# Optimization experiments

Hardware: AMD Instinct MI355X
Metric: run time of the kernel (lower is better)

## Reference

```python
import jax, jax.numpy as jnp
import numpy as np

N_STEPS = 5
STATE_DIM = 512
ANN_DIM = 256
N_NODES = 2048
N_EDGE_TYPES = 4


def setup_inputs() -> dict:
    key = jax.random.key(0)
    ks = jax.random.split(key, 12)
    D, E, N = STATE_DIM, N_EDGE_TYPES, N_NODES
    s = 0.02
    adjacency = (jax.random.uniform(ks[0], (N, N * 2 * E)) < 0.015).astype(jnp.float32)
    annotations = jax.random.normal(ks[1], (N, ANN_DIM), dtype=jnp.float32)
    W_prop = jax.random.normal(ks[2], (2 * E, D, D), dtype=jnp.float32) * s
    b_prop = jnp.zeros((2 * E, D), dtype=jnp.float32)
    Wz = jax.random.normal(ks[3], (D, D), dtype=jnp.float32) * s
    Uz = jax.random.normal(ks[4], (D, D), dtype=jnp.float32) * s
    bz = jnp.zeros((D,), dtype=jnp.float32)
    Wr = jax.random.normal(ks[5], (D, D), dtype=jnp.float32) * s
    Ur = jax.random.normal(ks[6], (D, D), dtype=jnp.float32) * s
    br = jnp.zeros((D,), dtype=jnp.float32)
    Wh = jax.random.normal(ks[7], (D, D), dtype=jnp.float32) * s
    Uh = jax.random.normal(ks[8], (D, D), dtype=jnp.float32) * s
    bh = jnp.zeros((D,), dtype=jnp.float32)
    return dict(adjacency=adjacency, annotations=annotations, W_prop=W_prop, b_prop=b_prop,
                Wz=Wz, Uz=Uz, bz=bz, Wr=Wr, Ur=Ur, br=br, Wh=Wh, Uh=Uh, bh=bh)


def reference(adjacency, annotations, W_prop, b_prop, Wz, Uz, bz, Wr, Ur, br, Wh, Uh, bh):
    N = annotations.shape[0]
    D = W_prop.shape[-1]
    # pad annotations into first columns of state (input1[:, :ann_dim] = annotations)
    h = jnp.zeros((N, D), dtype=annotations.dtype).at[:, :annotations.shape[1]].set(annotations)
    for _ in range(N_STEPS):
        # per-edge-type linear transforms: edge_type_list [2E, N, D]
        t = jnp.einsum('nd,edf->enf', h, W_prop) + b_prop[:, None, :]
        # adjacency aggregation: A is [N, N*2E] with per-edge-type column blocks
        a = adjacency @ t.reshape(-1, D)  # [N, D]
        # GRU node update (UpdateNet)
        z = jax.nn.sigmoid(a @ Wz + h @ Uz + bz)
        r = jax.nn.sigmoid(a @ Wr + h @ Ur + br)
        h_tilde = jnp.tanh(a @ Wh + (r * h) @ Uh + bh)
        h = (1.0 - z) * h + z * h_tilde
    return h
```

## Files before the change

### kernel.cpp

```cpp
#include <hip/hip_runtime.h>

typedef __attribute__((ext_vector_type(8))) short short8;
typedef __attribute__((ext_vector_type(4))) float floatx4;

#define NSTEPS 5
#define DD 512
#define ANN 256
#define NNODE 2048
#define NEDGE 8
#define NCOLS (NNODE * NEDGE)
#define MAXE 96
#define KP (NEDGE * DD)


typedef __attribute__((address_space(3))) unsigned lds_u32;
typedef const __attribute__((address_space(1))) unsigned g_u32;
__device__ __forceinline__ void gload16(const short* g, short* l) {
    __builtin_amdgcn_global_load_lds((g_u32*)g, (lds_u32*)l, 16, 0, 0);
}

__device__ inline float bf2f(unsigned short s) {
    unsigned u = ((unsigned)s) << 16;
    float f; __builtin_memcpy(&f, &u, 4);
    return f;
}
__device__ inline unsigned short f2bf(float f) {
    unsigned u; __builtin_memcpy(&u, &f, 4);
    u += 0x7fffu + ((u >> 16) & 1u);
    return (unsigned short)(u >> 16);
}
__device__ inline void split2(float x, unsigned short& hi, unsigned short& lo) {
    hi = f2bf(x);
    lo = f2bf(x - bf2f(hi));
}
__device__ inline void fo_write(short* __restrict__ Fhi, short* __restrict__ Flo,
                                int row, int col, float v) {
    unsigned short hs, ls;
    split2(v, hs, ls);
    size_t a = ((size_t)(row >> 4) * 64 + (col >> 3)) * 128 + ((row & 15) << 3) + (col & 7);
    Fhi[a] = (short)hs;
    Flo[a] = (short)ls;
}
__device__ inline void fo_write2(short* __restrict__ Fhi, short* __restrict__ Flo,
                                 int row, int c, float v0, float v1) {
    unsigned short h0, l0, h1, l1;
    split2(v0, h0, l0);
    split2(v1, h1, l1);
    size_t a = ((size_t)(row >> 4) * 64 + (c >> 3)) * 128 + ((row & 15) << 3) + (c & 7);
    *(unsigned*)(Fhi + a) = (unsigned)h0 | ((unsigned)h1 << 16);
    *(unsigned*)(Flo + a) = (unsigned)l0 | ((unsigned)l1 << 16);
}

__global__ __launch_bounds__(256) void k_init(const float* __restrict__ ann,
                                              float* __restrict__ h,
                                              short* __restrict__ HBhi,
                                              short* __restrict__ HBlo,
                                              int* __restrict__ cnt2) {
    int n = blockIdx.x, t = threadIdx.x;
    int c = 2 * t;
    float v0 = 0.f, v1 = 0.f;
    if (c < ANN) {
        v0 = ann[(size_t)n * ANN + c];
        v1 = ann[(size_t)n * ANN + c + 1];
    }
    h[(size_t)n * DD + c]     = v0;
    h[(size_t)n * DD + c + 1] = v1;
    fo_write2(HBhi, HBlo, n, c, v0, v1);
    if (t < NEDGE) cnt2[n * NEDGE + t] = 0;
}

__global__ __launch_bounds__(256) void k_build(const float* __restrict__ adj,
                                               int* __restrict__ cnt2,
                                               unsigned short* __restrict__ idx) {
    int n = blockIdx.x;
    const float* row = adj + (size_t)n * NCOLS;
    for (int j8 = threadIdx.x; j8 < NCOLS / 8; j8 += 256) {
        floatx4 a = *(const floatx4*)(row + j8 * 8);
        floatx4 b = *(const floatx4*)(row + j8 * 8 + 4);
        unsigned nz = 0;
        #pragma unroll
        for (int i = 0; i < 4; i++) {
            if (a[i] != 0.f) nz |= 1u << i;
            if (b[i] != 0.f) nz |= 1u << (4 + i);
        }
        while (nz) {
            int i = __builtin_ctz(nz);
            nz &= nz - 1;
            int j = j8 * 8 + i;
            int e = j >> 11;
            int m = j & (NNODE - 1);
            int p = atomicAdd(&cnt2[n * NEDGE + e], 1);
            if (p < MAXE) idx[((size_t)n * NEDGE + e) * MAXE + p] = (unsigned short)m;
        }
    }
}

__global__ __launch_bounds__(256) void k_transP(const float* __restrict__ W,
                                                short* __restrict__ Fhi,
                                                short* __restrict__ Flo, int K) {
    __shared__ float st[32][33];
    int tx = threadIdx.x & 31, ty = threadIdx.x >> 5;
    int k0 = blockIdx.x * 32, n0 = blockIdx.y * 32;
    #pragma unroll
    for (int i = 0; i < 4; i++)
        st[ty + i * 8][tx] = W[(size_t)(k0 + ty + i * 8) * DD + n0 + tx];
    __syncthreads();
    #pragma unroll
    for (int i = 0; i < 4; i++) {
        int n = n0 + ty + i * 8, k = k0 + tx;
        float v = st[tx][ty + i * 8];
        unsigned short hs, ls;
        split2(v, hs, ls);
        size_t a = ((size_t)(n >> 4) * (K >> 3) + (k >> 3)) * 128 + ((n & 15) << 3) + (k & 7);
        Fhi[a] = (short)hs;
        Flo[a] = (short)ls;
    }
}

__global__ __launch_bounds__(256) void k_transG(const float* __restrict__ s00,
                                                const float* __restrict__ s10,
                                                const float* __restrict__ s01,
                                                const float* __restrict__ s11,
                                                short* __restrict__ Fhi,
                                                short* __restrict__ Flo) {
    __shared__ float st[32][33];
    const int K = 2 * DD;
    int tx = threadIdx.x & 31, ty = threadIdx.x >> 5;
    int k0 = blockIdx.x * 32, n0 = blockIdx.y * 32;
    const float* sk0 = (n0 < DD) ? s00 : s01;
    const float* sk1 = (n0 < DD) ? s10 : s11;
    #pragma unroll
    for (int i = 0; i < 4; i++) {
        int k = k0 + ty + i * 8;
        const float* s = (k < DD) ? sk0 : sk1;
        st[ty + i * 8][tx] = s[(size_t)(k & (DD - 1)) * DD + ((n0 + tx) & (DD - 1))];
    }
    __syncthreads();
    #pragma unroll
    for (int i = 0; i < 4; i++) {
        int n = n0 + ty + i * 8, k = k0 + tx;
        float v = st[tx][ty + i * 8];
        unsigned short hs, ls;
        split2(v, hs, ls);
        size_t a = ((size_t)(n >> 4) * (K >> 3) + (k >> 3)) * 128 + ((n & 15) << 3) + (k & 7);
        Fhi[a] = (short)hs;
        Flo[a] = (short)ls;
    }
}

__global__ __launch_bounds__(256) void k_gather_all(const float* __restrict__ h,
                                                    const int* __restrict__ cnt2,
                                                    const unsigned short* __restrict__ idx,
                                                    const float* __restrict__ bp,
                                                    short* __restrict__ Gbhi,
                                                    short* __restrict__ Gblo,
                                                    float* __restrict__ abuf) {
    __shared__ unsigned short sidx[NEDGE * MAXE];
    __shared__ int scnt[NEDGE];
    int n = blockIdx.x, t = threadIdx.x;

    if (t < NEDGE) scnt[t] = cnt2[n * NEDGE + t];
    for (int j = t; j < NEDGE * MAXE / 2; j += 256)
        ((unsigned*)sidx)[j] = ((const unsigned*)(idx + (size_t)n * NEDGE * MAXE))[j];
    __syncthreads();

    const int th = t & 127;
    const int eg = t >> 7;
    size_t wbase = ((size_t)(n >> 4) * 512) * 128 + ((n & 15) << 3) + ((th & 1) << 2);

    #pragma unroll 1
    for (int ee = 0; ee < 4; ee++) {
        int e = eg * 4 + ee;
        int raw = scnt[e];
        int m = raw > MAXE ? MAXE : raw;
        const unsigned short* row = &sidx[e * MAXE];
        floatx4 a0 = (floatx4){0.f, 0.f, 0.f, 0.f};
        floatx4 a1 = (floatx4){0.f, 0.f, 0.f, 0.f};
        int i = 0;
        for (; i + 16 <= m; i += 16) {
            #pragma unroll
            for (int j = 0; j < 8; j++) {
                a0 += *(const floatx4*)(h + (size_t)row[i + j] * DD + 4 * th);
                a1 += *(const floatx4*)(h + (size_t)row[i + 8 + j] * DD + 4 * th);
            }
        }
        if (i + 8 <= m) {
            #pragma unroll
            for (int j = 0; j < 8; j++)
                a0 += *(const floatx4*)(h + (size_t)row[i + j] * DD + 4 * th);
            i += 8;
        }
        if (i + 4 <= m) {
            #pragma unroll
            for (int j = 0; j < 4; j++)
                a1 += *(const floatx4*)(h + (size_t)row[i + j] * DD + 4 * th);
            i += 4;
        }
        for (; i < m; i++)
            a0 += *(const floatx4*)(h + (size_t)row[i] * DD + 4 * th);
        floatx4 a = a0 + a1;

        unsigned short hs[4], ls[4];
        #pragma unroll
        for (int j = 0; j < 4; j++) split2(a[j], hs[j], ls[j]);
        unsigned long long hp = (unsigned long long)hs[0] | ((unsigned long long)hs[1] << 16)
                              | ((unsigned long long)hs[2] << 32) | ((unsigned long long)hs[3] << 48);
        unsigned long long lp = (unsigned long long)ls[0] | ((unsigned long long)ls[1] << 16)
                              | ((unsigned long long)ls[2] << 32) | ((unsigned long long)ls[3] << 48);
        size_t addr = wbase + (size_t)(e * 64 + (th >> 1)) * 128;
        __builtin_nontemporal_store(hp, (unsigned long long*)(Gbhi + addr));
        __builtin_nontemporal_store(lp, (unsigned long long*)(Gblo + addr));
    }

    if (eg == 0) {
        floatx4 s = (floatx4){0.f, 0.f, 0.f, 0.f};
        #pragma unroll
        for (int e = 0; e < NEDGE; e++)
            s += (float)scnt[e] * *(const floatx4*)(bp + e * DD + 4 * th);
        __builtin_nontemporal_store(s, (floatx4*)(abuf + (size_t)n * DD + 4 * th));
    }
}

template<int MODE>
__global__ __launch_bounds__(256, 4) void k_gemm8(
    const short* __restrict__ A0hi, const short* __restrict__ A0lo,
    const short* __restrict__ A1hi, const short* __restrict__ A1lo,
    const short* __restrict__ Bhi,  const short* __restrict__ Blo,
    const float* __restrict__ bias0, const float* __restrict__ bias1,
    float* __restrict__ zbuf,
    float* __restrict__ h,
    short* __restrict__ Ohi, short* __restrict__ Olo,
    float* __restrict__ P0, float* __restrict__ P1) {

    __shared__ short S[24][512];

    const int tid = threadIdx.x;
    const int lane = tid & 63;
    const int wave = tid >> 6;
    const int wm = wave >> 1;
    const int wn = wave & 1;
    const int quad = lane >> 4;
    const int l16 = lane & 15;

    const int pbid = blockIdx.x;
    const int x = pbid & 7;
    const int j = pbid >> 3;
    const int mband = x * 4 + (j & 3);
    int kh, bx;
    if (MODE == 1) { kh = 0; bx = j >> 2; }
    else           { kh = (j >> 2) & 1; bx = j >> 3; }
    const int blockM = mband * 64;
    const int blockN = bx * 32;
    const int mt0 = blockM >> 4, nt0 = blockN >> 4;
    const int KCB = (MODE == 0) ? 512 : 128;
    const int bko = (MODE == 0) ? kh * 256 : (MODE == 2 ? kh * 64 : 0);
    const int Kloc = (MODE == 0) ? 2048 : (MODE == 1 ? 1024 : 512);

    const short* Ahi_s = (MODE == 2 && kh) ? A1hi : A0hi;
    const short* Alo_s = (MODE == 2 && kh) ? A1lo : A0lo;

    floatx4 acc[2];
    acc[0] = (floatx4){0.f, 0.f, 0.f, 0.f};
    acc[1] = (floatx4){0.f, 0.f, 0.f, 0.f};

    auto gaddr = [&](int k0, int s) -> const short* {
        if (s < 16) {
            int pl = s >> 3, u = s & 7;
            int mt = u >> 1, ks = u & 1;
            const short* base;
            int kc, stride;
            if (MODE == 0) {
                base = pl ? A0lo : A0hi;
                kc = kh * 256 + (k0 >> 3) + ks * 4;
                stride = 512;
            } else if (MODE == 1) {
                int seg = k0 >> 9;
                base = seg ? (pl ? A1lo : A1hi) : (pl ? A0lo : A0hi);
                kc = ((k0 & 511) >> 3) + ks * 4;
                stride = 64;
            } else {
                base = pl ? Alo_s : Ahi_s;
                kc = (k0 >> 3) + ks * 4;
                stride = 64;
            }
            return base + ((size_t)(mt0 + mt) * stride + kc) * 128;
        } else {
            int u = s - 16, pl = u >> 2, ks = (u >> 1) & 1, nt = u & 1;
            const short* base = pl ? Blo : Bhi;
            return base + ((size_t)(nt0 + nt) * KCB + bko + (k0 >> 3) + ks * 4) * 128;
        }
    };

    for (int k0 = 0; k0 < Kloc; k0 += 64) {
        #pragma unroll
        for (int jj = 0; jj < 6; jj++) {
            int s = jj * 4 + wave;
            gload16(gaddr(k0, s) + lane * 8, &S[s][lane * 8]);
        }
        __syncthreads();

        #pragma unroll
        for (int ks = 0; ks < 2; ks++) {
            short8 ah[2], al[2], bh, bl;
            #pragma unroll
            for (int mi = 0; mi < 2; mi++) {
                ah[mi] = *(const short8*)&S[(wm * 2 + mi) * 2 + ks][lane * 8];
                al[mi] = *(const short8*)&S[8 + (wm * 2 + mi) * 2 + ks][lane * 8];
            }
            bh = *(const short8*)&S[16 + ks * 2 + wn][lane * 8];
            bl = *(const short8*)&S[20 + ks * 2 + wn][lane * 8];
            #pragma unroll
            for (int mi = 0; mi < 2; mi++) {
                acc[mi] = __builtin_amdgcn_mfma_f32_16x16x32_bf16(ah[mi], bh, acc[mi], 0, 0, 0);
                acc[mi] = __builtin_amdgcn_mfma_f32_16x16x32_bf16(ah[mi], bl, acc[mi], 0, 0, 0);
                acc[mi] = __builtin_amdgcn_mfma_f32_16x16x32_bf16(al[mi], bh, acc[mi], 0, 0, 0);
            }
        }
        __syncthreads();
    }

    float* P = kh ? P1 : P0;
    #pragma unroll
    for (int mi = 0; mi < 2; mi++) {
        int gcol = blockN + wn * 16 + l16;
        #pragma unroll
        for (int r = 0; r < 4; r++) {
            int grow = blockM + wm * 32 + mi * 16 + quad * 4 + r;
            float v = acc[mi][r];
            if (MODE == 0 || MODE == 2) {
                P[(size_t)grow * DD + gcol] = v;
            } else {
                if (gcol < DD) {
                    size_t o = (size_t)grow * DD + gcol;
                    zbuf[o] = 1.f / (1.f + __expf(-(v + bias0[gcol])));
                } else {
                    int c = gcol - DD;
                    size_t o = (size_t)grow * DD + c;
                    float rr = 1.f / (1.f + __expf(-(v + bias1[c])));
                    fo_write(Ohi, Olo, grow, c, rr * h[o]);
                }
            }
        }
    }
}

__global__ __launch_bounds__(256) void k_combP(const float* __restrict__ P0,
                                               const float* __restrict__ P1,
                                               const float* __restrict__ abuf,
                                               short* __restrict__ Gahi,
                                               short* __restrict__ Galo) {
    int n = blockIdx.x, t = threadIdx.x;
    size_t o = (size_t)n * DD + 2 * t;
    float v0 = P0[o] + P1[o] + abuf[o];
    float v1 = P0[o + 1] + P1[o + 1] + abuf[o + 1];
    fo_write2(Gahi, Galo, n, 2 * t, v0, v1);
}

__global__ __launch_bounds__(256) void k_combF(const float* __restrict__ P0,
                                               const float* __restrict__ P1,
                                               const float* __restrict__ bh,
                                               const float* __restrict__ zbuf,
                                               float* __restrict__ h,
                                               short* __restrict__ HBhi,
                                               short* __restrict__ HBlo,
                                               float* __restrict__ outF) {
    int n = blockIdx.x, t = threadIdx.x;
    int c = 2 * t;
    size_t o = (size_t)n * DD + c;
    float hn0, hn1;
    {
        float v = P0[o] + P1[o] + bh[c];
        hn0 = (1.f - zbuf[o]) * h[o] + zbuf[o] * tanhf(v);
    }
    {
        float v = P0[o + 1] + P1[o + 1] + bh[c + 1];
        hn1 = (1.f - zbuf[o + 1]) * h[o + 1] + zbuf[o + 1] * tanhf(v);
    }
    h[o] = hn0;
    h[o + 1] = hn1;
    fo_write2(HBhi, HBlo, n, c, hn0, hn1);
    outF[o] = hn0;
    outF[o + 1] = hn1;
}

extern "C" void kernel_launch(void* const* d_in, const int* in_sizes, int n_in,
                              void* d_out, int out_size, void* d_ws, size_t ws_size,
                              hipStream_t stream) {
    const float* adj = (const float*)d_in[0];
    const float* ann = (const float*)d_in[1];
    const float* Wp  = (const float*)d_in[2];
    const float* bp  = (const float*)d_in[3];
    const float* Wz  = (const float*)d_in[4];
    const float* Uz  = (const float*)d_in[5];
    const float* bz  = (const float*)d_in[6];
    const float* Wr  = (const float*)d_in[7];
    const float* Ur  = (const float*)d_in[8];
    const float* br  = (const float*)d_in[9];
    const float* Wh  = (const float*)d_in[10];
    const float* Uh  = (const float*)d_in[11];
    const float* bh  = (const float*)d_in[12];

    char* p = (char*)d_ws;
    float* h     = (float*)p; p += (size_t)NNODE * DD * 4;
    float* abuf  = (float*)p; p += (size_t)NNODE * DD * 4;
    float* P0    = (float*)p; p += (size_t)NNODE * DD * 4;
    float* P1    = (float*)p; p += (size_t)NNODE * DD * 4;
    short* Gbhi  = (short*)p; p += (size_t)NNODE * KP * 2;
    short* Gblo  = (short*)p; p += (size_t)NNODE * KP * 2;
    short* Gahi  = (short*)p; p += (size_t)NNODE * DD * 2;
    short* Galo  = (short*)p; p += (size_t)NNODE * DD * 2;
    short* HBhi  = (short*)p; p += (size_t)NNODE * DD * 2;
    short* HBlo  = (short*)p; p += (size_t)NNODE * DD * 2;
    short* RHhi  = (short*)p; p += (size_t)NNODE * DD * 2;
    short* RHlo  = (short*)p; p += (size_t)NNODE * DD * 2;
    short* WpThi = (short*)p; p += (size_t)DD * KP * 2;
    short* WpTlo = (short*)p; p += (size_t)DD * KP * 2;
    short* ZRhi  = (short*)p; p += (size_t)(2 * DD) * (2 * DD) * 2;
    short* ZRlo  = (short*)p; p += (size_t)(2 * DD) * (2 * DD) * 2;
    short* HThi  = (short*)p; p += (size_t)DD * (2 * DD) * 2;
    short* HTlo  = (short*)p; p += (size_t)DD * (2 * DD) * 2;
    unsigned short* idx = (unsigned short*)p;
    p += (size_t)NNODE * NEDGE * MAXE * 2;
    int* cnt2 = (int*)p; p += (size_t)NNODE * NEDGE * 4;

    float* outF = (float*)d_out;

    k_init<<<NNODE, 256, 0, stream>>>(ann, h, HBhi, HBlo, cnt2);
    k_build<<<NNODE, 256, 0, stream>>>(adj, cnt2, idx);
    k_transP<<<dim3(KP / 32, DD / 32), 256, 0, stream>>>(Wp, WpThi, WpTlo, KP);
    k_transG<<<dim3(32, 32), 256, 0, stream>>>(Wz, Uz, Wr, Ur, ZRhi, ZRlo);
    k_transG<<<dim3(32, 16), 256, 0, stream>>>(Wh, Uh, Wh, Uh, HThi, HTlo);

    for (int s = 0; s < NSTEPS; s++) {
        k_gather_all<<<NNODE, 256, 0, stream>>>(h, cnt2, idx, bp, Gbhi, Gblo, abuf);
        k_gemm8<0><<<1024, 256, 0, stream>>>(Gbhi, Gblo, nullptr, nullptr,
                                             WpThi, WpTlo, nullptr, nullptr,
                                             nullptr, nullptr, nullptr, nullptr, P0, P1);
        k_combP<<<NNODE, 256, 0, stream>>>(P0, P1, abuf, Gahi, Galo);
        k_gemm8<1><<<1024, 256, 0, stream>>>(Gahi, Galo, HBhi, HBlo,
                                             ZRhi, ZRlo, bz, br,
                                             abuf, h, RHhi, RHlo, nullptr, nullptr);
        k_gemm8<2><<<1024, 256, 0, stream>>>(Gahi, Galo, RHhi, RHlo,
                                             HThi, HTlo, nullptr, nullptr,
                                             nullptr, nullptr, nullptr, nullptr, P0, P1);
        k_combF<<<NNODE, 256, 0, stream>>>(P0, P1, bh, abuf, h, HBhi, HBlo, outF);
    }
}
```

Before: 1.049 ms.

## Split gather into half-edge blocks with padded zero-row indices and move bias into combP

The gather kernel now launches two blocks per node, each covering four edge types, with a block-to-node mapping that interleaves nodes across groups. Index lists are pre-filled with a sentinel that points to an added all-zero row of h. This lets the inner loop pad the count to a multiple of eight and load eight indices as one 16-byte vector, with no scalar tail handling. The per-edge bias sum moves from the gather into combP, which computes it from the counts. The aim is better occupancy and fewer branches on the memory-bound gather. The cost is extra loads of the zero row and a larger h buffer.

```diff
diff --git a/kernel.cpp b/kernel.cpp
--- a/kernel.cpp
+++ b/kernel.cpp
@@ -2,6 +2,7 @@
 
 typedef __attribute__((ext_vector_type(8))) short short8;
 typedef __attribute__((ext_vector_type(4))) float floatx4;
+typedef __attribute__((ext_vector_type(4))) unsigned uintx4;
 
 #define NSTEPS 5
 #define DD 512
@@ -55,7 +56,8 @@
                                               float* __restrict__ h,
                                               short* __restrict__ HBhi,
                                               short* __restrict__ HBlo,
-                                              int* __restrict__ cnt2) {
+                                              int* __restrict__ cnt2,
+                                              unsigned short* __restrict__ idx) {
     int n = blockIdx.x, t = threadIdx.x;
     int c = 2 * t;
     float v0 = 0.f, v1 = 0.f;
@@ -67,6 +69,13 @@
     h[(size_t)n * DD + c + 1] = v1;
     fo_write2(HBhi, HBlo, n, c, v0, v1);
     if (t < NEDGE) cnt2[n * NEDGE + t] = 0;
+    unsigned* ip = (unsigned*)(idx + (size_t)n * NEDGE * MAXE);
+    for (int j = t; j < NEDGE * MAXE / 2; j += 256)
+        ip[j] = 2048u | (2048u << 16);
+    if (n == 0) {
+        h[(size_t)NNODE * DD + c]     = 0.f;
+        h[(size_t)NNODE * DD + c + 1] = 0.f;
+    }
 }
 
 __global__ __launch_bounds__(256) void k_build(const float* __restrict__ adj,
@@ -151,73 +160,64 @@
 __global__ __launch_bounds__(256) void k_gather_all(const float* __restrict__ h,
                                                     const int* __restrict__ cnt2,
                                                     const unsigned short* __restrict__ idx,
-                                                    const float* __restrict__ bp,
                                                     short* __restrict__ Gbhi,
-                                                    short* __restrict__ Gblo,
-                                                    float* __restrict__ abuf) {
-    __shared__ unsigned short sidx[NEDGE * MAXE];
-    __shared__ int scnt[NEDGE];
-    int n = blockIdx.x, t = threadIdx.x;
-
-    if (t < NEDGE) scnt[t] = cnt2[n * NEDGE + t];
-    for (int j = t; j < NEDGE * MAXE / 2; j += 256)
-        ((unsigned*)sidx)[j] = ((const unsigned*)(idx + (size_t)n * NEDGE * MAXE))[j];
-    __syncthreads();
-
+                                                    short* __restrict__ Gblo) {
+    __shared__ unsigned short sidx[4 * MAXE];
+    __shared__ int scnt[4];
+    const int b = blockIdx.x;
+    const int x = b & 7;
+    const int u = b >> 3;
+    const int n = x * 256 + (u >> 1);
+    const int half = u & 1;
+    const int t = threadIdx.x;
     const int th = t & 127;
     const int eg = t >> 7;
+
+    if (t < 4) scnt[t] = cnt2[n * NEDGE + half * 4 + t];
+    {
+        const unsigned* src = (const unsigned*)(idx + ((size_t)n * NEDGE + half * 4) * MAXE);
+        if (t < 4 * MAXE / 2) ((unsigned*)sidx)[t] = src[t];
+    }
+    __syncthreads();
+
+    const float* hp = h + 4 * th;
     size_t wbase = ((size_t)(n >> 4) * 512) * 128 + ((n & 15) << 3) + ((th & 1) << 2);
 
     #pragma unroll 1
-    for (int ee = 0; ee < 4; ee++) {
-        int e = eg * 4 + ee;
-        int raw = scnt[e];
-        int m = raw > MAXE ? MAXE : raw;
-        const unsigned short* row = &sidx[e * MAXE];
+    for (int ee = 0; ee < 2; ee++) {
+        const int el = eg * 2 + ee;
+        const int ge = half * 4 + el;
+        int m = scnt[el];
+        m = m > MAXE ? MAXE : m;
+        m = (m + 7) & ~7;
+        const unsigned short* row = &sidx[el * MAXE];
         floatx4 a0 = (floatx4){0.f, 0.f, 0.f, 0.f};
         floatx4 a1 = (floatx4){0.f, 0.f, 0.f, 0.f};
-        int i = 0;
-        for (; i + 16 <= m; i += 16) {
-            #pragma unroll
-            for (int j = 0; j < 8; j++) {
-                a0 += *(const floatx4*)(h + (size_t)row[i + j] * DD + 4 * th);
-                a1 += *(const floatx4*)(h + (size_t)row[i + 8 + j] * DD + 4 * th);
-            }
-        }
-        if (i + 8 <= m) {
-            #pragma unroll
-            for (int j = 0; j < 8; j++)
-                a0 += *(const floatx4*)(h + (size_t)row[i + j] * DD + 4 * th);
-            i += 8;
-        }
-        if (i + 4 <= m) {
-            #pragma unroll
-            for (int j = 0; j < 4; j++)
-                a1 += *(const floatx4*)(h + (size_t)row[i + j] * DD + 4 * th);
-            i += 4;
-        }
-        for (; i < m; i++)
-            a0 += *(const floatx4*)(h + (size_t)row[i] * DD + 4 * th);
+        for (int i = 0; i < m; i += 8) {
+            uintx4 w = *(const uintx4*)(row + i);
+            floatx4 v0 = *(const floatx4*)(hp + (size_t)(w[0] & 0xffffu) * DD);
+            floatx4 v1 = *(const floatx4*)(hp + (size_t)(w[0] >> 16) * DD);
+            floatx4 v2 = *(const floatx4*)(hp + (size_t)(w[1] & 0xffffu) * DD);
+            floatx4 v3 = *(const floatx4*)(hp + (size_t)(w[1] >> 16) * DD);
+            floatx4 v4 = *(const floatx4*)(hp + (size_t)(w[2] & 0xffffu) * DD);
+            floatx4 v5 = *(const floatx4*)(hp + (size_t)(w[2] >> 16) * DD);
+            floatx4 v6 = *(const floatx4*)(hp + (size_t)(w[3] & 0xffffu) * DD);
+            floatx4 v7 = *(const floatx4*)(hp + (size_t)(w[3] >> 16) * DD);
+            a0 += v0; a1 += v1; a0 += v2; a1 += v3;
+            a0 += v4; a1 += v5; a0 += v6; a1 += v7;
+        }
         floatx4 a = a0 + a1;
 
         unsigned short hs[4], ls[4];
         #pragma unroll
         for (int j = 0; j < 4; j++) split2(a[j], hs[j], ls[j]);
-        unsigned long long hp = (unsigned long long)hs[0] | ((unsigned long long)hs[1] << 16)
-                              | ((unsigned long long)hs[2] << 32) | ((unsigned long long)hs[3] << 48);
-        unsigned long long lp = (unsigned long long)ls[0] | ((unsigned long long)ls[1] << 16)
-                              | ((unsigned long long)ls[2] << 32) | ((unsigned long long)ls[3] << 48);
-        size_t addr = wbase + (size_t)(e * 64 + (th >> 1)) * 128;
-        __builtin_nontemporal_store(hp, (unsigned long long*)(Gbhi + addr));
-        __builtin_nontemporal_store(lp, (unsigned long long*)(Gblo + addr));
-    }
-
-    if (eg == 0) {
-        floatx4 s = (floatx4){0.f, 0.f, 0.f, 0.f};
-        #pragma unroll
-        for (int e = 0; e < NEDGE; e++)
-            s += (float)scnt[e] * *(const floatx4*)(bp + e * DD + 4 * th);
-        __builtin_nontemporal_store(s, (floatx4*)(abuf + (size_t)n * DD + 4 * th));
+        unsigned long long hpk = (unsigned long long)hs[0] | ((unsigned long long)hs[1] << 16)
+                               | ((unsigned long long)hs[2] << 32) | ((unsigned long long)hs[3] << 48);
+        unsigned long long lpk = (unsigned long long)ls[0] | ((unsigned long long)ls[1] << 16)
+                               | ((unsigned long long)ls[2] << 32) | ((unsigned long long)ls[3] << 48);
+        size_t addr = wbase + (size_t)(ge * 64 + (th >> 1)) * 128;
+        __builtin_nontemporal_store(hpk, (unsigned long long*)(Gbhi + addr));
+        __builtin_nontemporal_store(lpk, (unsigned long long*)(Gblo + addr));
     }
 }
 
@@ -346,14 +346,23 @@
 
 __global__ __launch_bounds__(256) void k_combP(const float* __restrict__ P0,
                                                const float* __restrict__ P1,
-                                               const float* __restrict__ abuf,
+                                               const int* __restrict__ cnt2,
+                                               const float* __restrict__ bp,
                                                short* __restrict__ Gahi,
                                                short* __restrict__ Galo) {
     int n = blockIdx.x, t = threadIdx.x;
-    size_t o = (size_t)n * DD + 2 * t;
-    float v0 = P0[o] + P1[o] + abuf[o];
-    float v1 = P0[o + 1] + P1[o + 1] + abuf[o + 1];
-    fo_write2(Gahi, Galo, n, 2 * t, v0, v1);
+    int c = 2 * t;
+    float s0 = 0.f, s1 = 0.f;
+    #pragma unroll
+    for (int e = 0; e < NEDGE; e++) {
+        float ce = (float)cnt2[n * NEDGE + e];
+        s0 += ce * bp[e * DD + c];
+        s1 += ce * bp[e * DD + c + 1];
+    }
+    size_t o = (size_t)n * DD + c;
+    float v0 = P0[o] + P1[o] + s0;
+    float v1 = P0[o + 1] + P1[o + 1] + s1;
+    fo_write2(Gahi, Galo, n, c, v0, v1);
 }
 
 __global__ __launch_bounds__(256) void k_combF(const float* __restrict__ P0,
@@ -401,7 +410,7 @@
     const float* bh  = (const float*)d_in[12];
 
     char* p = (char*)d_ws;
-    float* h     = (float*)p; p += (size_t)NNODE * DD * 4;
+    float* h     = (float*)p; p += (size_t)(NNODE + 1) * DD * 4;
     float* abuf  = (float*)p; p += (size_t)NNODE * DD * 4;
     float* P0    = (float*)p; p += (size_t)NNODE * DD * 4;
     float* P1    = (float*)p; p += (size_t)NNODE * DD * 4;
@@ -425,18 +434,18 @@
 
     float* outF = (float*)d_out;
 
-    k_init<<<NNODE, 256, 0, stream>>>(ann, h, HBhi, HBlo, cnt2);
+    k_init<<<NNODE, 256, 0, stream>>>(ann, h, HBhi, HBlo, cnt2, idx);
     k_build<<<NNODE, 256, 0, stream>>>(adj, cnt2, idx);
     k_transP<<<dim3(KP / 32, DD / 32), 256, 0, stream>>>(Wp, WpThi, WpTlo, KP);
     k_transG<<<dim3(32, 32), 256, 0, stream>>>(Wz, Uz, Wr, Ur, ZRhi, ZRlo);
     k_transG<<<dim3(32, 16), 256, 0, stream>>>(Wh, Uh, Wh, Uh, HThi, HTlo);
 
     for (int s = 0; s < NSTEPS; s++) {
-        k_gather_all<<<NNODE, 256, 0, stream>>>(h, cnt2, idx, bp, Gbhi, Gblo, abuf);
+        k_gather_all<<<2 * NNODE, 256, 0, stream>>>(h, cnt2, idx, Gbhi, Gblo);
         k_gemm8<0><<<1024, 256, 0, stream>>>(Gbhi, Gblo, nullptr, nullptr,
                                              WpThi, WpTlo, nullptr, nullptr,
                                              nullptr, nullptr, nullptr, nullptr, P0, P1);
-        k_combP<<<NNODE, 256, 0, stream>>>(P0, P1, abuf, Gahi, Galo);
+        k_combP<<<NNODE, 256, 0, stream>>>(P0, P1, cnt2, bp, Gahi, Galo);
         k_gemm8<1><<<1024, 256, 0, stream>>>(Gahi, Galo, HBhi, HBlo,
                                              ZRhi, ZRlo, bz, br,
                                              abuf, h, RHhi, RHlo, nullptr, nullptr);
```

New measurement: 1.125 ms. 1.07x slower.
